# Optimization experiments

Measured on AMD Instinct MI355X. Metric: run time of the kernel, lower is better.

## Reference

```python
import jax, jax.numpy as jnp
import numpy as np

D_MODEL = 256
NHEAD = 8
NUM_LAYERS = 4
LN_EPS = 1e-5

def _layernorm(x, g, b):
    mu = jnp.mean(x, axis=-1, keepdims=True)
    var = jnp.mean((x - mu) ** 2, axis=-1, keepdims=True)
    return (x - mu) * jax.lax.rsqrt(var + LN_EPS) * g + b

def setup_inputs() -> dict:
    key = jax.random.key(0)
    ks = jax.random.split(key, 16)
    B, M, D, L = 2, 2048, D_MODEL, NUM_LAYERS
    s = 0.02
    inp = {
        'x': jax.random.normal(ks[0], (B, M, D), jnp.float32),
        'coords': jax.random.normal(ks[1], (B, M, 3), jnp.float32),
        'wq': jax.random.normal(ks[2], (L, D, D), jnp.float32) * s,
        'bq': jnp.zeros((L, D), jnp.float32),
        'wk': jax.random.normal(ks[3], (L, D, D), jnp.float32) * s,
        'bk': jnp.zeros((L, D), jnp.float32),
        'wv': jax.random.normal(ks[4], (L, D, D), jnp.float32) * s,
        'bv': jnp.zeros((L, D), jnp.float32),
        'alpha': jnp.full((L,), 0.1, jnp.float32),
        'w1': jax.random.normal(ks[5], (L, D, 2 * D), jnp.float32) * s,
        'b1': jnp.zeros((L, 2 * D), jnp.float32),
        'w2': jax.random.normal(ks[6], (L, 2 * D, D), jnp.float32) * s,
        'b2': jnp.zeros((L, D), jnp.float32),
        'ln1_g': jnp.ones((L, D), jnp.float32),
        'ln1_b': jnp.zeros((L, D), jnp.float32),
        'ln2_g': jnp.ones((L, D), jnp.float32),
        'ln2_b': jnp.zeros((L, D), jnp.float32),
    }
    return inp

def reference(x, coords, wq, bq, wk, bk, wv, bv, alpha, w1, b1, w2, b2, ln1_g, ln1_b, ln2_g, ln2_b):
    B, M, D = x.shape
    H = NHEAD
    dk = D // H
    # Geometric bias: per-batch block of the original B*M x B*M dot matrix,
    # i.e. G[b] = coords[b] @ coords[b].T  (identical math, computed directly).
    G0 = jnp.einsum('bmd,bnd->bmn', coords, coords)  # [B, M, M]
    scale = 1.0 / jnp.sqrt(jnp.asarray(dk, x.dtype))

    def heads(t):  # [B,M,D] -> [B,H,M,dk]
        return t.reshape(B, M, H, dk).transpose(0, 2, 1, 3)

    for i in range(NUM_LAYERS):
        q = heads(x @ wq[i] + bq[i])
        k = heads(x @ wk[i] + bk[i])
        v = heads(x @ wv[i] + bv[i])
        scores = jnp.einsum('bhmd,bhnd->bhmn', q, k) * scale + (alpha[i] * G0)[:, None]
        attn = jax.nn.softmax(scores, axis=-1)
        out = jnp.einsum('bhmn,bhnd->bhmd', attn, v)
        out = out.transpose(0, 2, 1, 3).reshape(B, M, D)
        x = _layernorm(x + out, ln1_g[i], ln1_b[i])
        ff = jax.nn.relu(x @ w1[i] + b1[i]) @ w2[i] + b2[i]
        x = _layernorm(x + ff, ln2_g[i], ln2_b[i])
    return x
```

## Files before the change

kernel.cpp:

```cpp
#include <hip/hip_runtime.h>

typedef unsigned short u16;
typedef __attribute__((ext_vector_type(8))) short short8;
typedef __attribute__((ext_vector_type(4))) float f32x4;
typedef __attribute__((ext_vector_type(4))) u16 u16x4;

#define MFMA16(a, b, c) __builtin_amdgcn_mfma_f32_16x16x32_bf16(a, b, c, 0, 0, 0)

#define LOG2E 1.4426950408889634f
#define QSCALE 0.25506038410312156f

__device__ __forceinline__ u16 f2bf(float f) {
    unsigned int u = __builtin_bit_cast(unsigned int, f);
    u += 0x7fffu + ((u >> 16) & 1u);
    return (u16)(u >> 16);
}

__global__ __launch_bounds__(256) void repack_kernel(
    const float* __restrict__ wq, const float* __restrict__ wk, const float* __restrict__ wv,
    const float* __restrict__ bq, const float* __restrict__ bk, const float* __restrict__ bv,
    const float* __restrict__ w1, const float* __restrict__ w2,
    u16* __restrict__ wqkvT, u16* __restrict__ w1T, u16* __restrict__ w2T,
    float* __restrict__ bqkv)
{
    long idx = (long)blockIdx.x * 256 + threadIdx.x;
    const long NQ = 4L * 768 * 256;
    const long N1 = 4L * 512 * 256;
    const long N2 = 4L * 256 * 512;
    const long NB = 4L * 768;
    if (idx < NQ) {
        long l = idx / (768 * 256); long r = idx % (768 * 256);
        long n = r / 256, k = r % 256;
        float v;
        if (n < 256)      v = wq[(l * 256 + k) * 256 + n] * QSCALE;
        else if (n < 512) v = wk[(l * 256 + k) * 256 + (n - 256)];
        else              v = wv[(l * 256 + k) * 256 + (n - 512)];
        wqkvT[idx] = f2bf(v);
    } else if ((idx -= NQ) < N1) {
        long l = idx / (512 * 256); long r = idx % (512 * 256);
        long n = r / 256, k = r % 256;
        w1T[idx] = f2bf(w1[(l * 256 + k) * 512 + n]);
    } else if ((idx -= N1) < N2) {
        long l = idx / (256 * 512); long r = idx % (256 * 512);
        long n = r / 512, k = r % 512;
        w2T[idx] = f2bf(w2[(l * 512 + k) * 256 + n]);
    } else if ((idx -= N2) < NB) {
        long l = idx / 768; long n = idx % 768;
        float v = (n < 256) ? bq[l * 256 + n] * QSCALE
                : (n < 512) ? bk[l * 256 + (n - 256)]
                            : bv[l * 256 + (n - 512)];
        bqkv[l * 768 + n] = v;
    }
}

__global__ __launch_bounds__(256) void xconv_kernel(
    const float* __restrict__ xin, const float* __restrict__ coords,
    float* __restrict__ xf, u16* __restrict__ xb, u16* __restrict__ kcoord)
{
    long idx = (long)blockIdx.x * 256 + threadIdx.x;
    if (idx < 4096L * 256) {
        float v = xin[idx];
        xf[idx] = v;
        xb[idx] = f2bf(v);
    }
    if (idx < 4096) {
        const float* c = coords + idx * 3;
        u16 r0 = f2bf(c[0] * LOG2E), r1 = f2bf(c[1] * LOG2E), r2 = f2bf(c[2] * LOG2E);
        uint4 lo; lo.x = (unsigned)r0 | ((unsigned)r1 << 16); lo.y = (unsigned)r2; lo.z = 0; lo.w = 0;
        uint4 z4; z4.x = 0; z4.y = 0; z4.z = 0; z4.w = 0;
        uint4* dst = (uint4*)(kcoord + idx * 32);
        dst[0] = lo; dst[1] = z4; dst[2] = z4; dst[3] = z4;
    }
}

__global__ __launch_bounds__(256) void qkvgemm_kernel(
    const u16* __restrict__ A, const u16* __restrict__ BT,
    const float* __restrict__ bias,
    u16* __restrict__ qt, u16* __restrict__ kt, u16* __restrict__ vt)
{
    const int K = 256;
    int w = threadIdx.x >> 6, lane = threadIdx.x & 63;
    int wr = w >> 1, wc = w & 1;
    int m0 = blockIdx.x * 64 + wr * 32;
    int n0 = blockIdx.y * 64 + wc * 32;
    int l16 = lane & 15, lhi = lane >> 4;

    f32x4 acc[2][2];
#pragma unroll
    for (int i = 0; i < 2; i++)
#pragma unroll
        for (int j = 0; j < 2; j++) acc[i][j] = (f32x4){0.f, 0.f, 0.f, 0.f};

    const u16* Ap = A + (size_t)(m0 + l16) * K + lhi * 8;
    const u16* Bp = BT + (size_t)(n0 + l16) * K + lhi * 8;

#pragma unroll 2
    for (int k = 0; k < K; k += 32) {
        short8 a0 = *(const short8*)(Ap + k);
        short8 a1 = *(const short8*)(Ap + (size_t)16 * K + k);
        short8 b0 = *(const short8*)(Bp + k);
        short8 b1 = *(const short8*)(Bp + (size_t)16 * K + k);
        acc[0][0] = MFMA16(a0, b0, acc[0][0]);
        acc[0][1] = MFMA16(a0, b1, acc[0][1]);
        acc[1][0] = MFMA16(a1, b0, acc[1][0]);
        acc[1][1] = MFMA16(a1, b1, acc[1][1]);
    }

#pragma unroll
    for (int i = 0; i < 2; i++)
#pragma unroll
        for (int j = 0; j < 2; j++) {
            int n = n0 + j * 16 + l16;
            float bs = bias[n];
            int sect = n >> 8;
            int h = (n >> 5) & 7;
            int d = n & 31;
            int m = m0 + i * 16 + lhi * 4;
            int b = m >> 11, mseq = m & 2047;
            if (sect < 2) {
                u16* dst = (sect == 0 ? qt : kt) + ((size_t)(b * 8 + h) * 2048 + mseq) * 32 + d;
#pragma unroll
                for (int r = 0; r < 4; r++) dst[(size_t)r * 32] = f2bf(acc[i][j][r] + bs);
            } else {
                u16x4 pk;
#pragma unroll
                for (int r = 0; r < 4; r++) pk[r] = f2bf(acc[i][j][r] + bs);
                *(u16x4*)(vt + ((size_t)(b * 8 + h) * 32 + d) * 2048 + mseq) = pk;
            }
        }
}

template <bool RELU, bool OUTF32>
__global__ __launch_bounds__(256) void gemm_kernel(
    const u16* __restrict__ A, const u16* __restrict__ BT,
    const float* __restrict__ bias, void* __restrict__ outp,
    int M, int N, int K)
{
    int w = threadIdx.x >> 6, lane = threadIdx.x & 63;
    int wr = w >> 1, wc = w & 1;
    int m0 = blockIdx.x * 64 + wr * 32;
    int n0 = blockIdx.y * 64 + wc * 32;
    int l16 = lane & 15, lhi = lane >> 4;

    f32x4 acc[2][2];
#pragma unroll
    for (int i = 0; i < 2; i++)
#pragma unroll
        for (int j = 0; j < 2; j++) acc[i][j] = (f32x4){0.f, 0.f, 0.f, 0.f};

    const u16* Ap = A + (size_t)(m0 + l16) * K + lhi * 8;
    const u16* Bp = BT + (size_t)(n0 + l16) * K + lhi * 8;

#pragma unroll 2
    for (int k = 0; k < K; k += 32) {
        short8 a0 = *(const short8*)(Ap + k);
        short8 a1 = *(const short8*)(Ap + (size_t)16 * K + k);
        short8 b0 = *(const short8*)(Bp + k);
        short8 b1 = *(const short8*)(Bp + (size_t)16 * K + k);
        acc[0][0] = MFMA16(a0, b0, acc[0][0]);
        acc[0][1] = MFMA16(a0, b1, acc[0][1]);
        acc[1][0] = MFMA16(a1, b0, acc[1][0]);
        acc[1][1] = MFMA16(a1, b1, acc[1][1]);
    }

#pragma unroll
    for (int i = 0; i < 2; i++)
#pragma unroll
        for (int j = 0; j < 2; j++) {
            int n = n0 + j * 16 + l16;
            float bs = bias[n];
#pragma unroll
            for (int r = 0; r < 4; r++) {
                int m = m0 + i * 16 + lhi * 4 + r;
                float v = acc[i][j][r] + bs;
                if (RELU) v = fmaxf(v, 0.f);
                if (OUTF32) ((float*)outp)[(size_t)m * N + n] = v;
                else        ((u16*)outp)[(size_t)m * N + n] = f2bf(v);
            }
        }
}

__global__ __launch_bounds__(256, 4) void attn_kernel(
    const u16* __restrict__ qt, const u16* __restrict__ kt, const u16* __restrict__ vt,
    const u16* __restrict__ kcoord, const float* __restrict__ coords,
    const float* __restrict__ alpha, int layer, float* __restrict__ outp)
{
    int tid = threadIdx.x;
    int w = tid >> 6, lane = tid & 63;
    int flat = blockIdx.x;
    int bh = (flat & 7) | (((flat >> 3) & 1) << 3);
    int b = bh >> 3, h = bh & 7;
    int m0 = (flat >> 4) * 32;
    int l16 = lane & 15, lhi = lane >> 4;

    __shared__ __align__(16) char smem[18432 + 1024];
    float* olds = (float*)smem;
    float* mlds = (float*)(smem + 18432);

    const u16* qbase = qt + (size_t)bh * 2048 * 32;
    float al = alpha[layer];
    short8 qlo[2], qhi[2];
#pragma unroll
    for (int qq = 0; qq < 2; qq++) {
        qlo[qq] = *(const short8*)(qbase + (size_t)(m0 + qq * 16 + l16) * 32 + lhi * 8);
        short8 z = {0, 0, 0, 0, 0, 0, 0, 0};
        qhi[qq] = z;
        if (lhi == 0) {
            const float* c = coords + (size_t)(b * 2048 + m0 + qq * 16 + l16) * 3;
            qhi[qq][0] = (short)f2bf(c[0] * al);
            qhi[qq][1] = (short)f2bf(c[1] * al);
            qhi[qq][2] = (short)f2bf(c[2] * al);
        }
    }

    f32x4 oacc[2][2];
#pragma unroll
    for (int qq = 0; qq < 2; qq++)
#pragma unroll
        for (int dt = 0; dt < 2; dt++) oacc[qq][dt] = (f32x4){0.f, 0.f, 0.f, 0.f};
    float mrow[2] = {-1e30f, -1e30f}, lrow[2] = {0.f, 0.f};

    const u16* kb  = kt + (size_t)bh * 2048 * 32 + lhi * 8;
    const u16* kcb = kcoord + (size_t)b * 2048 * 32 + lhi * 8;
    const u16* vbase = vt + ((size_t)bh * 32 + l16) * 2048;

    for (int nb = w * 8; nb < w * 8 + 8; nb++) {
        int n0b = nb * 64;
        f32x4 s[2][4];
#pragma unroll
        for (int t = 0; t < 4; t++) {
            size_t nr = (size_t)(n0b + t * 16 + l16);
            short8 klo = *(const short8*)(kb + nr * 32);
            short8 khi = *(const short8*)(kcb + nr * 32);
            f32x4 z0 = (f32x4){0.f, 0.f, 0.f, 0.f};
            z0 = MFMA16(klo, qlo[0], z0);
            s[0][t] = MFMA16(khi, qhi[0], z0);
            f32x4 z1 = (f32x4){0.f, 0.f, 0.f, 0.f};
            z1 = MFMA16(klo, qlo[1], z1);
            s[1][t] = MFMA16(khi, qhi[1], z1);
        }
#pragma unroll
        for (int qq = 0; qq < 2; qq++) {
            float tm = -1e30f;
#pragma unroll
            for (int t = 0; t < 4; t++) {
                float a = fmaxf(fmaxf(s[qq][t][0], s[qq][t][1]), fmaxf(s[qq][t][2], s[qq][t][3]));
                tm = fmaxf(tm, a);
            }
            tm = fmaxf(tm, __shfl_xor(tm, 16, 64));
            tm = fmaxf(tm, __shfl_xor(tm, 32, 64));
            float mnew = fmaxf(mrow[qq], tm);
            float corr = exp2f(mrow[qq] - mnew);
            mrow[qq] = mnew;
#pragma unroll
            for (int dt = 0; dt < 2; dt++)
#pragma unroll
                for (int r = 0; r < 4; r++) oacc[qq][dt][r] *= corr;

            float rs = 0.f;
#pragma unroll
            for (int t = 0; t < 4; t++) {
#pragma unroll
                for (int r = 0; r < 4; r++) s[qq][t][r] = exp2f(s[qq][t][r] - mrow[qq]);
                rs += (s[qq][t][0] + s[qq][t][1]) + (s[qq][t][2] + s[qq][t][3]);
            }
            rs += __shfl_xor(rs, 16, 64);
            rs += __shfl_xor(rs, 32, 64);
            lrow[qq] = lrow[qq] * corr + rs;

            u16* pl = (u16*)smem + (w * 2 + qq) * 1024;
#pragma unroll
            for (int t = 0; t < 4; t++) {
                unsigned p0, p1;
                asm("v_cvt_pk_bf16_f32 %0, %1, %2" : "=v"(p0) : "v"(s[qq][t][0]), "v"(s[qq][t][1]));
                asm("v_cvt_pk_bf16_f32 %0, %1, %2" : "=v"(p1) : "v"(s[qq][t][2]), "v"(s[qq][t][3]));
                int slot = (t * 2 + (lhi >> 1)) ^ (l16 & 7);
                uint2 val; val.x = p0; val.y = p1;
                *(uint2*)(pl + l16 * 64 + (slot << 3) + (lhi & 1) * 4) = val;
            }
        }
        asm volatile("s_waitcnt lgkmcnt(0)" ::: "memory");
        __builtin_amdgcn_sched_barrier(0);

        u16* pl0 = (u16*)smem + (w * 2) * 1024;
        u16* pl1 = (u16*)smem + (w * 2 + 1) * 1024;
#pragma unroll
        for (int kk = 0; kk < 2; kk++) {
            int soff = ((kk * 4 + lhi) ^ (l16 & 7)) << 3;
            short8 pf0 = *(const short8*)(pl0 + l16 * 64 + soff);
            short8 pf1 = *(const short8*)(pl1 + l16 * 64 + soff);
#pragma unroll
            for (int dt = 0; dt < 2; dt++) {
                short8 vf = *(const short8*)(vbase + (size_t)dt * 16 * 2048 + n0b + kk * 32 + lhi * 8);
                oacc[0][dt] = MFMA16(vf, pf0, oacc[0][dt]);
                oacc[1][dt] = MFMA16(vf, pf1, oacc[1][dt]);
            }
        }
    }

    __syncthreads();
    if (lhi == 0) {
#pragma unroll
        for (int qq = 0; qq < 2; qq++) {
            mlds[((w * 2 + qq) * 2 + 0) * 16 + l16] = mrow[qq];
            mlds[((w * 2 + qq) * 2 + 1) * 16 + l16] = lrow[qq];
        }
    }
#pragma unroll
    for (int qq = 0; qq < 2; qq++)
#pragma unroll
        for (int dt = 0; dt < 2; dt++)
            *(f32x4*)(olds + ((size_t)(w * 2 + qq) * 16 + l16) * 36 + dt * 16 + lhi * 4) = oacc[qq][dt];
    __syncthreads();

    int d = tid & 31, q8 = tid >> 5;
#pragma unroll
    for (int qq2 = 0; qq2 < 4; qq2++) {
        int q = q8 + qq2 * 8;
        int q16 = q & 15, qh2 = q >> 4;
        float mw[4], lw[4];
#pragma unroll
        for (int ww = 0; ww < 4; ww++) {
            mw[ww] = mlds[((ww * 2 + qh2) * 2 + 0) * 16 + q16];
            lw[ww] = mlds[((ww * 2 + qh2) * 2 + 1) * 16 + q16];
        }
        float mg = fmaxf(fmaxf(mw[0], mw[1]), fmaxf(mw[2], mw[3]));
        float o = 0.f, lg = 0.f;
#pragma unroll
        for (int ww = 0; ww < 4; ww++) {
            float sc = exp2f(mw[ww] - mg);
            lg += lw[ww] * sc;
            o += olds[((size_t)(ww * 2 + qh2) * 16 + q16) * 36 + d] * sc;
        }
        outp[(size_t)(b * 2048 + m0 + q) * 256 + h * 32 + d] = o / lg;
    }
}

__global__ __launch_bounds__(256) void ln_kernel(
    const float* __restrict__ xin, const float* __restrict__ add,
    const float* __restrict__ g, const float* __restrict__ bb,
    float* __restrict__ outf, u16* __restrict__ outb)
{
    int w = threadIdx.x >> 6, lane = threadIdx.x & 63;
    int row = blockIdx.x * 4 + w;
    size_t base = (size_t)row * 256 + lane * 4;
    float4 xv = *(const float4*)(xin + base);
    float4 av = *(const float4*)(add + base);
    float s0 = xv.x + av.x, s1 = xv.y + av.y, s2 = xv.z + av.z, s3 = xv.w + av.w;
    float sum = s0 + s1 + s2 + s3;
    float sq = s0 * s0 + s1 * s1 + s2 * s2 + s3 * s3;
#pragma unroll
    for (int off = 1; off < 64; off <<= 1) {
        sum += __shfl_xor(sum, off, 64);
        sq += __shfl_xor(sq, off, 64);
    }
    float mu = sum * (1.f / 256.f);
    float var = sq * (1.f / 256.f) - mu * mu;
    float rs = rsqrtf(var + 1e-5f);
    float4 gv = *(const float4*)(g + lane * 4);
    float4 bv = *(const float4*)(bb + lane * 4);
    float y0 = (s0 - mu) * rs * gv.x + bv.x;
    float y1 = (s1 - mu) * rs * gv.y + bv.y;
    float y2 = (s2 - mu) * rs * gv.z + bv.z;
    float y3 = (s3 - mu) * rs * gv.w + bv.w;
    float4 yo; yo.x = y0; yo.y = y1; yo.z = y2; yo.w = y3;
    *(float4*)(outf + base) = yo;
    unsigned int p0 = (unsigned int)f2bf(y0) | ((unsigned int)f2bf(y1) << 16);
    unsigned int p1 = (unsigned int)f2bf(y2) | ((unsigned int)f2bf(y3) << 16);
    uint2 pk; pk.x = p0; pk.y = p1;
    *(uint2*)(outb + base) = pk;
}

extern "C" void kernel_launch(void* const* d_in, const int* in_sizes, int n_in,
                              void* d_out, int out_size, void* d_ws, size_t ws_size,
                              hipStream_t stream)
{
    const float* x_in   = (const float*)d_in[0];
    const float* coords = (const float*)d_in[1];
    const float* wq = (const float*)d_in[2];
    const float* bq = (const float*)d_in[3];
    const float* wk = (const float*)d_in[4];
    const float* bk = (const float*)d_in[5];
    const float* wv = (const float*)d_in[6];
    const float* bv = (const float*)d_in[7];
    const float* alpha = (const float*)d_in[8];
    const float* w1 = (const float*)d_in[9];
    const float* b1 = (const float*)d_in[10];
    const float* w2 = (const float*)d_in[11];
    const float* b2 = (const float*)d_in[12];
    const float* ln1g = (const float*)d_in[13];
    const float* ln1b = (const float*)d_in[14];
    const float* ln2g = (const float*)d_in[15];
    const float* ln2b = (const float*)d_in[16];
    float* out = (float*)d_out;

    char* ws = (char*)d_ws;
    size_t off = 0;
    auto alloc = [&](size_t bytes) -> void* {
        void* p = ws + off;
        off += (bytes + 255) & ~(size_t)255;
        return p;
    };
    float* x_f32 = (float*)alloc(4096UL * 256 * 4);
    u16*   x_bf  = (u16*)  alloc(4096UL * 256 * 2);
    u16*   qt    = (u16*)  alloc(16UL * 2048 * 32 * 2);
    u16*   ktp   = (u16*)  alloc(16UL * 2048 * 32 * 2);
    u16*   vtp   = (u16*)  alloc(16UL * 32 * 2048 * 2);
    u16*   kcoord= (u16*)  alloc(2UL * 2048 * 32 * 2);
    float* attnb = (float*)alloc(4096UL * 256 * 4);
    u16*   mid   = (u16*)  alloc(4096UL * 512 * 2);
    float* ffn   = (float*)alloc(4096UL * 256 * 4);
    u16*   wqkvT = (u16*)  alloc(4UL * 768 * 256 * 2);
    u16*   w1T   = (u16*)  alloc(4UL * 512 * 256 * 2);
    u16*   w2T   = (u16*)  alloc(4UL * 256 * 512 * 2);
    float* bqkv  = (float*)alloc(4UL * 768 * 4);

    repack_kernel<<<7180, 256, 0, stream>>>(wq, wk, wv, bq, bk, bv, w1, w2,
                                            wqkvT, w1T, w2T, bqkv);
    xconv_kernel<<<4096, 256, 0, stream>>>(x_in, coords, x_f32, x_bf, kcoord);

    for (int i = 0; i < 4; i++) {
        qkvgemm_kernel<<<dim3(64, 12), 256, 0, stream>>>(
            x_bf, wqkvT + (size_t)i * 768 * 256, bqkv + i * 768, qt, ktp, vtp);
        attn_kernel<<<1024, 256, 0, stream>>>(qt, ktp, vtp, kcoord, coords, alpha, i, attnb);
        ln_kernel<<<1024, 256, 0, stream>>>(x_f32, attnb, ln1g + i * 256, ln1b + i * 256,
                                            x_f32, x_bf);
        gemm_kernel<true, false><<<dim3(64, 8), 256, 0, stream>>>(
            x_bf, w1T + (size_t)i * 512 * 256, b1 + i * 512, mid, 4096, 512, 256);
        gemm_kernel<false, true><<<dim3(64, 4), 256, 0, stream>>>(
            mid, w2T + (size_t)i * 256 * 512, b2 + i * 256, ffn, 4096, 256, 512);
        ln_kernel<<<1024, 256, 0, stream>>>(x_f32, ffn, ln2g + i * 256, ln2b + i * 256,
                                            (i == 3) ? out : x_f32, x_bf);
    }
}
```

Baseline: 335.7 us.

## Split attention KV range across two blocks and merge partials in layernorm

```diff
diff --git a/kernel.cpp b/kernel.cpp
--- a/kernel.cpp
+++ b/kernel.cpp
@@ -180,17 +180,19 @@
         }
 }
 
-__global__ __launch_bounds__(256, 4) void attn_kernel(
+__global__ __launch_bounds__(256, 8) void attn_kernel(
     const u16* __restrict__ qt, const u16* __restrict__ kt, const u16* __restrict__ vt,
     const u16* __restrict__ kcoord, const float* __restrict__ coords,
-    const float* __restrict__ alpha, int layer, float* __restrict__ outp)
+    const float* __restrict__ alpha, int layer,
+    float* __restrict__ po, float* __restrict__ pml)
 {
     int tid = threadIdx.x;
     int w = tid >> 6, lane = tid & 63;
     int flat = blockIdx.x;
     int bh = (flat & 7) | (((flat >> 3) & 1) << 3);
     int b = bh >> 3, h = bh & 7;
-    int m0 = (flat >> 4) * 32;
+    int m0 = ((flat >> 4) & 63) * 32;
+    int kvhalf = flat >> 10;
     int l16 = lane & 15, lhi = lane >> 4;
 
     __shared__ __align__(16) char smem[18432 + 1024];
@@ -224,7 +226,8 @@
     const u16* kcb = kcoord + (size_t)b * 2048 * 32 + lhi * 8;
     const u16* vbase = vt + ((size_t)bh * 32 + l16) * 2048;
 
-    for (int nb = w * 8; nb < w * 8 + 8; nb++) {
+    int nbase = kvhalf * 16 + w * 4;
+    for (int nb = nbase; nb < nbase + 4; nb++) {
         int n0b = nb * 64;
         f32x4 s[2][4];
 #pragma unroll
@@ -249,13 +252,16 @@
             }
             tm = fmaxf(tm, __shfl_xor(tm, 16, 64));
             tm = fmaxf(tm, __shfl_xor(tm, 32, 64));
-            float mnew = fmaxf(mrow[qq], tm);
-            float corr = exp2f(mrow[qq] - mnew);
-            mrow[qq] = mnew;
-#pragma unroll
-            for (int dt = 0; dt < 2; dt++)
-#pragma unroll
-                for (int r = 0; r < 4; r++) oacc[qq][dt][r] *= corr;
+            if (!__all(tm <= mrow[qq] + 8.f)) {
+                float mnew = fmaxf(mrow[qq], tm);
+                float corr = exp2f(mrow[qq] - mnew);
+                mrow[qq] = mnew;
+#pragma unroll
+                for (int dt = 0; dt < 2; dt++)
+#pragma unroll
+                    for (int r = 0; r < 4; r++) oacc[qq][dt][r] *= corr;
+                lrow[qq] *= corr;
+            }
 
             float rs = 0.f;
 #pragma unroll
@@ -266,7 +272,7 @@
             }
             rs += __shfl_xor(rs, 16, 64);
             rs += __shfl_xor(rs, 32, 64);
-            lrow[qq] = lrow[qq] * corr + rs;
+            lrow[qq] += rs;
 
             u16* pl = (u16*)smem + (w * 2 + qq) * 1024;
 #pragma unroll
@@ -332,8 +338,63 @@
             lg += lw[ww] * sc;
             o += olds[((size_t)(ww * 2 + qh2) * 16 + q16) * 36 + d] * sc;
         }
-        outp[(size_t)(b * 2048 + m0 + q) * 256 + h * 32 + d] = o / lg;
-    }
+        size_t row = (size_t)(b * 2048 + m0 + q);
+        po[((size_t)kvhalf * 4096 + row) * 256 + h * 32 + d] = o;
+        if (d == 0) {
+            float2 ml2; ml2.x = mg; ml2.y = lg;
+            *(float2*)(pml + ((size_t)kvhalf * 4096 + row) * 16 + h * 2) = ml2;
+        }
+    }
+}
+
+__global__ __launch_bounds__(256) void lnmerge_kernel(
+    const float* __restrict__ xin, const float* __restrict__ po,
+    const float* __restrict__ pml,
+    const float* __restrict__ g, const float* __restrict__ bb,
+    float* __restrict__ outf, u16* __restrict__ outb)
+{
+    int w = threadIdx.x >> 6, lane = threadIdx.x & 63;
+    int row = blockIdx.x * 4 + w;
+    int h = lane >> 3;
+    float m0v = pml[(size_t)row * 16 + h * 2];
+    float l0v = pml[(size_t)row * 16 + h * 2 + 1];
+    float m1v = pml[((size_t)4096 + row) * 16 + h * 2];
+    float l1v = pml[((size_t)4096 + row) * 16 + h * 2 + 1];
+    float mg = fmaxf(m0v, m1v);
+    float w0 = exp2f(m0v - mg), w1 = exp2f(m1v - mg);
+    float inv = 1.f / (l0v * w0 + l1v * w1);
+
+    size_t base = (size_t)row * 256 + lane * 4;
+    float4 xv = *(const float4*)(xin + base);
+    float4 a0 = *(const float4*)(po + base);
+    float4 a1 = *(const float4*)(po + (size_t)4096 * 256 + base);
+    float s0 = xv.x + (a0.x * w0 + a1.x * w1) * inv;
+    float s1 = xv.y + (a0.y * w0 + a1.y * w1) * inv;
+    float s2 = xv.z + (a0.z * w0 + a1.z * w1) * inv;
+    float s3 = xv.w + (a0.w * w0 + a1.w * w1) * inv;
+
+    float sum = s0 + s1 + s2 + s3;
+    float sq = s0 * s0 + s1 * s1 + s2 * s2 + s3 * s3;
+#pragma unroll
+    for (int off = 1; off < 64; off <<= 1) {
+        sum += __shfl_xor(sum, off, 64);
+        sq += __shfl_xor(sq, off, 64);
+    }
+    float mu = sum * (1.f / 256.f);
+    float var = sq * (1.f / 256.f) - mu * mu;
+    float rs = rsqrtf(var + 1e-5f);
+    float4 gv = *(const float4*)(g + lane * 4);
+    float4 bv = *(const float4*)(bb + lane * 4);
+    float y0 = (s0 - mu) * rs * gv.x + bv.x;
+    float y1 = (s1 - mu) * rs * gv.y + bv.y;
+    float y2 = (s2 - mu) * rs * gv.z + bv.z;
+    float y3 = (s3 - mu) * rs * gv.w + bv.w;
+    float4 yo; yo.x = y0; yo.y = y1; yo.z = y2; yo.w = y3;
+    *(float4*)(outf + base) = yo;
+    unsigned int p0 = (unsigned int)f2bf(y0) | ((unsigned int)f2bf(y1) << 16);
+    unsigned int p1 = (unsigned int)f2bf(y2) | ((unsigned int)f2bf(y3) << 16);
+    uint2 pk; pk.x = p0; pk.y = p1;
+    *(uint2*)(outb + base) = pk;
 }
 
 __global__ __launch_bounds__(256) void ln_kernel(
@@ -407,7 +468,8 @@
     u16*   ktp   = (u16*)  alloc(16UL * 2048 * 32 * 2);
     u16*   vtp   = (u16*)  alloc(16UL * 32 * 2048 * 2);
     u16*   kcoord= (u16*)  alloc(2UL * 2048 * 32 * 2);
-    float* attnb = (float*)alloc(4096UL * 256 * 4);
+    float* po    = (float*)alloc(2UL * 4096 * 256 * 4);
+    float* pml   = (float*)alloc(2UL * 4096 * 16 * 4);
     u16*   mid   = (u16*)  alloc(4096UL * 512 * 2);
     float* ffn   = (float*)alloc(4096UL * 256 * 4);
     u16*   wqkvT = (u16*)  alloc(4UL * 768 * 256 * 2);
@@ -422,9 +484,9 @@
     for (int i = 0; i < 4; i++) {
         qkvgemm_kernel<<<dim3(64, 12), 256, 0, stream>>>(
             x_bf, wqkvT + (size_t)i * 768 * 256, bqkv + i * 768, qt, ktp, vtp);
-        attn_kernel<<<1024, 256, 0, stream>>>(qt, ktp, vtp, kcoord, coords, alpha, i, attnb);
-        ln_kernel<<<1024, 256, 0, stream>>>(x_f32, attnb, ln1g + i * 256, ln1b + i * 256,
-                                            x_f32, x_bf);
+        attn_kernel<<<2048, 256, 0, stream>>>(qt, ktp, vtp, kcoord, coords, alpha, i, po, pml);
+        lnmerge_kernel<<<1024, 256, 0, stream>>>(x_f32, po, pml, ln1g + i * 256, ln1b + i * 256,
+                                                 x_f32, x_bf);
         gemm_kernel<true, false><<<dim3(64, 8), 256, 0, stream>>>(
             x_bf, w1T + (size_t)i * 512 * 256, b1 + i * 512, mid, 4096, 512, 256);
         gemm_kernel<false, true><<<dim3(64, 4), 256, 0, stream>>>(
```

New measurement: 530.9 us. 58.2% more time.
